# Kernel optimization log

Hardware: AMD Instinct MI355X
Metric: run time of the kernel (lower is better)

The kernel has to match this reference:

```python
import jax, jax.numpy as jnp
import numpy as np

D_MODEL = 1024
N_HEADS = 16
D_K = D_MODEL // N_HEADS


def setup_inputs() -> dict:
    key = jax.random.key(0)
    ks = jax.random.split(key, 12)
    B, S = 2, 2048
    scale = 1.0 / np.sqrt(D_MODEL)
    inp = {
        "query": jax.random.normal(ks[0], (B, S, D_MODEL), jnp.float32),
        "key": jax.random.normal(ks[1], (B, S, D_MODEL), jnp.float32),
        "value": jax.random.normal(ks[2], (B, S, D_MODEL), jnp.float32),
        "weights": jax.random.uniform(ks[3], (B, S), jnp.float32),
        "wq": jax.random.normal(ks[4], (D_MODEL, D_MODEL), jnp.float32) * scale,
        "bq": jnp.zeros((D_MODEL,), jnp.float32),
        "wk": jax.random.normal(ks[5], (D_MODEL, D_MODEL), jnp.float32) * scale,
        "bk": jnp.zeros((D_MODEL,), jnp.float32),
        "wv": jax.random.normal(ks[6], (D_MODEL, D_MODEL), jnp.float32) * scale,
        "bv": jnp.zeros((D_MODEL,), jnp.float32),
        "wo": jax.random.normal(ks[7], (D_MODEL, D_MODEL), jnp.float32) * scale,
        "bo": jnp.zeros((D_MODEL,), jnp.float32),
    }
    return inp


def _split_heads(x):
    # (B, S, d_model) -> (B, H, S, d_k)
    B, S, _ = x.shape
    return x.reshape(B, S, N_HEADS, D_K).transpose(0, 2, 1, 3)


def reference(query, key, value, weights, wq, bq, wk, bk, wv, bv, wo, bo):
    Q = _split_heads(query @ wq + bq)
    K = _split_heads(key @ wk + bk)
    V = _split_heads(value @ wv + bv)
    # scores: (B, H, n_q, n_kv)
    scores = jnp.einsum("bhqd,bhkd->bhqk", Q, K) / np.sqrt(D_K)
    log_w = jnp.log(weights + 1e-20)[:, None, None, :]  # (B,1,1,n_kv)
    attn = jax.nn.softmax(scores + log_w, axis=-1)
    out = jnp.einsum("bhqk,bhkd->bhqd", attn, V)
    B, H, S, Dk = out.shape
    out = out.transpose(0, 2, 1, 3).reshape(B, S, D_MODEL)
    return out @ wo + bo
```

## Files before the change

### kernel.cpp

```cpp
#include <hip/hip_runtime.h>

typedef unsigned short u16;
typedef __bf16 bf16x8 __attribute__((ext_vector_type(8)));
typedef float f32x4 __attribute__((ext_vector_type(4)));
typedef float f32x16 __attribute__((ext_vector_type(16)));

#define D_MODEL 1024
#define NH 16
#define DKD 64
#define BB 2
#define SS 2048
#define QSCL 0.18033688011112042f

#if __has_builtin(__builtin_amdgcn_exp2f)
#define EXP2(x) __builtin_amdgcn_exp2f(x)
#else
#define EXP2(x) exp2f(x)
#endif

__device__ __forceinline__ u16 f2bf(float f) {
  union { float f; unsigned u; } x; x.f = f;
  unsigned r = x.u + 0x7fffu + ((x.u >> 16) & 1u);
  return (u16)(r >> 16);
}

__device__ __forceinline__ void gld16(const u16* g, u16* l) {
  __builtin_amdgcn_global_load_lds((__attribute__((address_space(1))) void*)(g),
                                   (__attribute__((address_space(3))) void*)(l),
                                   16, 0, 0);
}

extern "C" __global__ void __launch_bounds__(256) kprep_conv(
    const float* __restrict__ q, const float* __restrict__ k, const float* __restrict__ v,
    const float* __restrict__ wts,
    u16* __restrict__ xq, u16* __restrict__ xk, u16* __restrict__ xv,
    float* __restrict__ lw)
{
  int z = blockIdx.y;
  if (blockIdx.x == 4096) {
    if (z == 0) {
      int i = threadIdx.x * 16;
      #pragma unroll
      for (int j = 0; j < 16; j += 4) {
        float4 val = *(const float4*)(wts + i + j);
        lw[i + j + 0] = log2f(val.x + 1e-20f) - 16.0f;
        lw[i + j + 1] = log2f(val.y + 1e-20f) - 16.0f;
        lw[i + j + 2] = log2f(val.z + 1e-20f) - 16.0f;
        lw[i + j + 3] = log2f(val.w + 1e-20f) - 16.0f;
      }
    }
    return;
  }
  const float* s = z == 0 ? q : (z == 1 ? k : v);
  u16* d = z == 0 ? xq : (z == 1 ? xk : xv);
  int i = (blockIdx.x * 256 + threadIdx.x) * 4;
  float4 val = *(const float4*)(s + i);
  ushort4 o;
  o.x = f2bf(val.x); o.y = f2bf(val.y); o.z = f2bf(val.z); o.w = f2bf(val.w);
  *(ushort4*)(d + i) = o;
}

extern "C" __global__ void __launch_bounds__(256) kprep_wt(
    const float* __restrict__ w0, const float* __restrict__ w1,
    const float* __restrict__ w2, const float* __restrict__ w3,
    u16* __restrict__ o0, u16* __restrict__ o1, u16* __restrict__ o2, u16* __restrict__ o3)
{
  const float* src; u16* dst;
  switch (blockIdx.z) {
    case 0: src = w0; dst = o0; break;
    case 1: src = w1; dst = o1; break;
    case 2: src = w2; dst = o2; break;
    default: src = w3; dst = o3; break;
  }
  __shared__ float t[32][33];
  int n0 = blockIdx.x * 32, k0 = blockIdx.y * 32;
  int tx = threadIdx.x & 31, ty = threadIdx.x >> 5;
  #pragma unroll
  for (int i = 0; i < 32; i += 8)
    t[ty + i][tx] = src[(k0 + ty + i) * D_MODEL + n0 + tx];
  __syncthreads();
  #pragma unroll
  for (int i = 0; i < 32; i += 8)
    dst[(size_t)(n0 + ty + i) * D_MODEL + k0 + tx] = f2bf(t[tx][ty + i]);
}

extern "C" __global__ void __launch_bounds__(256) ktrans_v(
    const u16* __restrict__ src, u16* __restrict__ dst)
{
  __shared__ u16 T[64][72];
  int bh = blockIdx.y; int s0 = blockIdx.x * 64;
  int tid = threadIdx.x;
  int r = tid >> 3, c = (tid & 7) * 8;
  #pragma unroll
  for (int i = 0; i < 2; ++i)
    *(bf16x8*)&T[r + i * 32][c] = *(const bf16x8*)&src[((size_t)bh * SS + s0 + r + i * 32) * DKD + c];
  __syncthreads();
  #pragma unroll
  for (int i = 0; i < 2; ++i) {
    int dk = r + i * 32;
    ushort4 o0, o1;
    o0.x = T[c + 0][dk]; o0.y = T[c + 1][dk]; o0.z = T[c + 2][dk]; o0.w = T[c + 3][dk];
    o1.x = T[c + 4][dk]; o1.y = T[c + 5][dk]; o1.z = T[c + 6][dk]; o1.w = T[c + 7][dk];
    *(ushort4*)&dst[((size_t)bh * DKD + dk) * SS + s0 + c] = o0;
    *(ushort4*)&dst[((size_t)bh * DKD + dk) * SS + s0 + c + 4] = o1;
  }
}

__device__ __forceinline__ void gemm_tile(const u16* __restrict__ Ag, const u16* __restrict__ Bg,
                                          u16* As, u16* Bs, f32x4 acc[4][4], int tid)
{
  int lane = tid & 63;
  int lr = lane & 15, lg = lane >> 4;
  int w = tid >> 6, wr = w >> 1, wc = w & 1;
  int sr7 = lr & 7;
  for (int k0 = 0; k0 < D_MODEL; k0 += 64) {
    #pragma unroll
    for (int c = 0; c < 4; ++c) {
      int idx = tid + c * 256;
      int row = idx >> 3, c3 = idx & 7;
      int col = (c3 ^ (row & 7)) * 8;
      gld16(Ag + row * D_MODEL + k0 + col, As + idx * 8);
      gld16(Bg + row * D_MODEL + k0 + col, Bs + idx * 8);
    }
    __syncthreads();
    #pragma unroll
    for (int kk = 0; kk < 2; ++kk) {
      bf16x8 af[4], bfr[4];
      #pragma unroll
      for (int mi = 0; mi < 4; ++mi)
        af[mi] = *(const bf16x8*)(As + (wr * 64 + mi * 16 + lr) * 64 + (((kk * 4 + lg) ^ sr7) * 8));
      #pragma unroll
      for (int nj = 0; nj < 4; ++nj)
        bfr[nj] = *(const bf16x8*)(Bs + (wc * 64 + nj * 16 + lr) * 64 + (((kk * 4 + lg) ^ sr7) * 8));
      #pragma unroll
      for (int mi = 0; mi < 4; ++mi)
        #pragma unroll
        for (int nj = 0; nj < 4; ++nj)
          acc[mi][nj] = __builtin_amdgcn_mfma_f32_16x16x32_bf16(af[mi], bfr[nj], acc[mi][nj], 0, 0, 0);
    }
    __syncthreads();
  }
}

extern "C" __global__ void __launch_bounds__(256) kgemm_qkv(
    const u16* __restrict__ xq, const u16* __restrict__ xk, const u16* __restrict__ xv,
    const u16* __restrict__ wqt, const u16* __restrict__ wkt, const u16* __restrict__ wvt,
    const float* __restrict__ bq, const float* __restrict__ bk, const float* __restrict__ bv,
    u16* __restrict__ Qb, u16* __restrict__ Kb, u16* __restrict__ Vb)
{
  __shared__ u16 As[128 * 64], Bs[128 * 64];
  int z = blockIdx.z;
  const u16* X  = z == 0 ? xq : (z == 1 ? xk : xv);
  const u16* Wt = z == 0 ? wqt : (z == 1 ? wkt : wvt);
  const float* bias = z == 0 ? bq : (z == 1 ? bk : bv);
  u16* dst = z == 0 ? Qb : (z == 1 ? Kb : Vb);
  int tid = threadIdx.x;
  f32x4 zero = {0.f, 0.f, 0.f, 0.f};
  f32x4 acc[4][4];
  #pragma unroll
  for (int i = 0; i < 4; ++i)
    #pragma unroll
    for (int j = 0; j < 4; ++j) acc[i][j] = zero;
  int m0 = blockIdx.y * 128, n0 = blockIdx.x * 128;
  gemm_tile(X + (size_t)m0 * D_MODEL, Wt + (size_t)n0 * D_MODEL, As, Bs, acc, tid);
  int lane = tid & 63, lr = lane & 15, lg = lane >> 4;
  int w = tid >> 6, wr = w >> 1, wc = w & 1;
  float scl = (z == 0) ? QSCL : 1.0f;
  #pragma unroll
  for (int mi = 0; mi < 4; ++mi)
    #pragma unroll
    for (int nj = 0; nj < 4; ++nj) {
      int n = n0 + wc * 64 + nj * 16 + lr;
      float bs = bias[n];
      int h = n >> 6, dk = n & 63;
      #pragma unroll
      for (int j = 0; j < 4; ++j) {
        int m = m0 + wr * 64 + mi * 16 + lg * 4 + j;
        int b = m >> 11, s = m & 2047;
        dst[(((size_t)(b * NH + h)) * SS + s) * DKD + dk] = f2bf((acc[mi][nj][j] + bs) * scl);
      }
    }
}

extern "C" __global__ void __launch_bounds__(256) kgemm_o(
    const u16* __restrict__ AO, const u16* __restrict__ wot,
    const float* __restrict__ bo, float* __restrict__ out)
{
  __shared__ u16 As[64 * 64], Bs[128 * 64];
  int tid = threadIdx.x;
  int lane = tid & 63, lr = lane & 15, lg = lane >> 4;
  int w = tid >> 6, wr = w & 1, wc = w >> 1;
  int sr7 = lr & 7;
  int m0 = blockIdx.y * 64, n0 = blockIdx.x * 128;
  const u16* Ag = AO + (size_t)m0 * D_MODEL;
  const u16* Bg = wot + (size_t)n0 * D_MODEL;
  f32x4 zero = {0.f, 0.f, 0.f, 0.f};
  f32x4 acc[2][4];
  #pragma unroll
  for (int i = 0; i < 2; ++i)
    #pragma unroll
    for (int j = 0; j < 4; ++j) acc[i][j] = zero;

  for (int k0 = 0; k0 < D_MODEL; k0 += 64) {
    #pragma unroll
    for (int c = 0; c < 2; ++c) {
      int idx = tid + c * 256;
      int row = idx >> 3, c3 = idx & 7;
      int col = (c3 ^ (row & 7)) * 8;
      gld16(Ag + row * D_MODEL + k0 + col, As + idx * 8);
    }
    #pragma unroll
    for (int c = 0; c < 4; ++c) {
      int idx = tid + c * 256;
      int row = idx >> 3, c3 = idx & 7;
      int col = (c3 ^ (row & 7)) * 8;
      gld16(Bg + row * D_MODEL + k0 + col, Bs + idx * 8);
    }
    __syncthreads();
    #pragma unroll
    for (int kk = 0; kk < 2; ++kk) {
      bf16x8 af[2], bfr[4];
      #pragma unroll
      for (int mi = 0; mi < 2; ++mi)
        af[mi] = *(const bf16x8*)(As + (wr * 32 + mi * 16 + lr) * 64 + (((kk * 4 + lg) ^ sr7) * 8));
      #pragma unroll
      for (int nj = 0; nj < 4; ++nj)
        bfr[nj] = *(const bf16x8*)(Bs + (wc * 64 + nj * 16 + lr) * 64 + (((kk * 4 + lg) ^ sr7) * 8));
      #pragma unroll
      for (int mi = 0; mi < 2; ++mi)
        #pragma unroll
        for (int nj = 0; nj < 4; ++nj)
          acc[mi][nj] = __builtin_amdgcn_mfma_f32_16x16x32_bf16(af[mi], bfr[nj], acc[mi][nj], 0, 0, 0);
    }
    __syncthreads();
  }

  #pragma unroll
  for (int mi = 0; mi < 2; ++mi)
    #pragma unroll
    for (int nj = 0; nj < 4; ++nj) {
      int n = n0 + wc * 64 + nj * 16 + lr;
      float bs = bo[n];
      #pragma unroll
      for (int j = 0; j < 4; ++j) {
        int m = m0 + wr * 32 + mi * 16 + lg * 4 + j;
        out[(size_t)m * D_MODEL + n] = acc[mi][nj][j] + bs;
      }
    }
}

extern "C" __global__ void __launch_bounds__(512, 4) kattn(
    const u16* __restrict__ Qb, const u16* __restrict__ Kb, const u16* __restrict__ Vt,
    const float* __restrict__ lw2, u16* __restrict__ AO)
{
  __shared__ __align__(16) char smem[2 * 16384 + 8192];
  float* lwf = (float*)(smem + 32768);

  int tid = threadIdx.x, lane = tid & 63, w = tid >> 6;
  int lq = lane & 31, hi = lane >> 5;
  int qw = w & 3, par = w >> 2;

  int n = blockIdx.x;
  int xcd = n & 7, slot = n >> 3;
  int bh = xcd + 8 * (slot >> 4);
  int q0 = (slot & 15) * 128;
  int b = bh >> 4, h = bh & 15;

  const u16* Qg = Qb + ((size_t)bh * SS + q0 + qw * 32) * DKD;
  const u16* Kg = Kb + (size_t)bh * SS * DKD;
  const u16* Vg = Vt + (size_t)bh * DKD * SS;
  const float* lwb = lw2 + b * SS;

  *(float4*)&lwf[tid * 4] = *(const float4*)(lwb + tid * 4);

  bf16x8 qf[4];
  #pragma unroll
  for (int kc = 0; kc < 4; ++kc)
    qf[kc] = *(const bf16x8*)(Qg + lq * DKD + kc * 16 + hi * 8);

  f32x16 acco[2] = {};
  float lsp[4] = {0.f, 0.f, 0.f, 0.f};

  int srow = tid >> 3, sc = ((tid & 7) ^ (srow & 7)) * 8;

#define KSLOT(sl) ((u16*)(smem + (sl) * 16384))
#define VSLOT(sl) ((u16*)(smem + (sl) * 16384 + 8192))
#define STAGE(t, sl) do { \
    gld16(Kg + (size_t)((t) * 64 + srow) * DKD + sc, KSLOT(sl) + tid * 8); \
    gld16(Vg + (size_t)srow * SS + (t) * 64 + sc, VSLOT(sl) + tid * 8); \
  } while (0)

  const u16* Kp = KSLOT(par);
  const u16* Vp = VSLOT(par);

  STAGE(0, 0); STAGE(1, 1);
  for (int i = 0; i < 16; ++i) {
    asm volatile("s_waitcnt vmcnt(0) lgkmcnt(0)" ::: "memory");
    __builtin_amdgcn_s_barrier();
    __builtin_amdgcn_sched_barrier(0);

    int t = 2 * i + par;
    int kv0 = t * 64;

    f32x16 st[2];
    #pragma unroll
    for (int nh = 0; nh < 2; ++nh)
      #pragma unroll
      for (int g = 0; g < 4; ++g) {
        f32x4 lv = *(const f32x4*)&lwf[kv0 + nh * 32 + 4 * hi + 8 * g];
        st[nh][4 * g + 0] = lv[0]; st[nh][4 * g + 1] = lv[1];
        st[nh][4 * g + 2] = lv[2]; st[nh][4 * g + 3] = lv[3];
      }

    __builtin_amdgcn_s_setprio(1);
    #pragma unroll
    for (int kc = 0; kc < 4; ++kc) {
      bf16x8 kf0 = *(const bf16x8*)&Kp[(lq) * 64      + (((kc * 2 + hi) ^ (lq & 7)) * 8)];
      bf16x8 kf1 = *(const bf16x8*)&Kp[(32 + lq) * 64 + (((kc * 2 + hi) ^ (lq & 7)) * 8)];
      st[0] = __builtin_amdgcn_mfma_f32_32x32x16_bf16(kf0, qf[kc], st[0], 0, 0, 0);
      st[1] = __builtin_amdgcn_mfma_f32_32x32x16_bf16(kf1, qf[kc], st[1], 0, 0, 0);
    }
    __builtin_amdgcn_s_setprio(0);

    unsigned wd[2][8];
    #pragma unroll
    for (int nh = 0; nh < 2; ++nh)
      #pragma unroll
      for (int r2 = 0; r2 < 8; ++r2) {
        float plo = EXP2(st[nh][2 * r2]);
        float phi = EXP2(st[nh][2 * r2 + 1]);
        lsp[r2 & 3] += plo + phi;
        union { unsigned u; __bf16 b2[2]; } cv;
        cv.b2[0] = (__bf16)plo; cv.b2[1] = (__bf16)phi;
        wd[nh][r2] = cv.u;
      }

    bf16x8 Pb[4];
    #pragma unroll
    for (int c = 0; c < 4; ++c) {
      int nh = c >> 1, j0 = 4 * (c & 1);
      auto s1 = __builtin_amdgcn_permlane32_swap(wd[nh][j0 + 0], wd[nh][j0 + 2], false, false);
      auto s2 = __builtin_amdgcn_permlane32_swap(wd[nh][j0 + 1], wd[nh][j0 + 3], false, false);
      union { unsigned u[4]; bf16x8 v; } pb;
      pb.u[0] = s1[0]; pb.u[1] = s2[0]; pb.u[2] = s1[1]; pb.u[3] = s2[1];
      Pb[c] = pb.v;
    }

    __builtin_amdgcn_s_setprio(1);
    #pragma unroll
    for (int c = 0; c < 4; ++c) {
      bf16x8 vf0 = *(const bf16x8*)&Vp[(lq) * 64      + (((c * 2 + hi) ^ (lq & 7)) * 8)];
      bf16x8 vf1 = *(const bf16x8*)&Vp[(32 + lq) * 64 + (((c * 2 + hi) ^ (lq & 7)) * 8)];
      acco[0] = __builtin_amdgcn_mfma_f32_32x32x16_bf16(vf0, Pb[c], acco[0], 0, 0, 0);
      acco[1] = __builtin_amdgcn_mfma_f32_32x32x16_bf16(vf1, Pb[c], acco[1], 0, 0, 0);
    }
    __builtin_amdgcn_s_setprio(0);

    __builtin_amdgcn_sched_barrier(0);
    __builtin_amdgcn_s_barrier();
    int tn = 2 * i + 2;
    if (tn < 32) { STAGE(tn, 0); STAGE(tn + 1, 1); }
  }
#undef STAGE

  float lsum_part = (lsp[0] + lsp[1]) + (lsp[2] + lsp[3]);
  float* comb = (float*)smem;
  int coff = (qw * 64 + lane) * 34;
  if (par == 1) {
    #pragma unroll
    for (int d = 0; d < 2; ++d)
      #pragma unroll
      for (int g = 0; g < 8; ++g)
        *(float2*)&comb[coff + (d * 8 + g) * 2] = make_float2(acco[d][2 * g], acco[d][2 * g + 1]);
    comb[coff + 32] = lsum_part;
  }
  __syncthreads();
  if (par == 0) {
    #pragma unroll
    for (int d = 0; d < 2; ++d)
      #pragma unroll
      for (int g = 0; g < 8; ++g) {
        float2 v = *(const float2*)&comb[coff + (d * 8 + g) * 2];
        acco[d][2 * g] += v.x; acco[d][2 * g + 1] += v.y;
      }
    lsum_part += comb[coff + 32];
    float lsum = lsum_part + __shfl_xor(lsum_part, 32);
    float inv = 1.0f / lsum;
    int s = q0 + qw * 32 + lq;
    size_t base = ((size_t)b * SS + s) * D_MODEL + h * DKD;
    #pragma unroll
    for (int dh = 0; dh < 2; ++dh)
      #pragma unroll
      for (int g = 0; g < 4; ++g) {
        ushort4 o;
        o.x = f2bf(acco[dh][4 * g + 0] * inv);
        o.y = f2bf(acco[dh][4 * g + 1] * inv);
        o.z = f2bf(acco[dh][4 * g + 2] * inv);
        o.w = f2bf(acco[dh][4 * g + 3] * inv);
        *(ushort4*)(AO + base + dh * 32 + 4 * hi + 8 * g) = o;
      }
  }
#undef KSLOT
#undef VSLOT
}

extern "C" void kernel_launch(void* const* d_in, const int* in_sizes, int n_in,
                              void* d_out, int out_size, void* d_ws, size_t ws_size,
                              hipStream_t stream) {
  const float* query = (const float*)d_in[0];
  const float* key_  = (const float*)d_in[1];
  const float* value = (const float*)d_in[2];
  const float* wts   = (const float*)d_in[3];
  const float* wq = (const float*)d_in[4];
  const float* bq = (const float*)d_in[5];
  const float* wk = (const float*)d_in[6];
  const float* bk = (const float*)d_in[7];
  const float* wv = (const float*)d_in[8];
  const float* bv = (const float*)d_in[9];
  const float* wo = (const float*)d_in[10];
  const float* bo = (const float*)d_in[11];
  float* out = (float*)d_out;

  char* ws = (char*)d_ws;
  const size_t MB = 1024 * 1024;
  u16* Xq  = (u16*)(ws + 0 * MB);
  u16* Xk  = (u16*)(ws + 8 * MB);
  u16* Xv  = (u16*)(ws + 16 * MB);
  u16* WqT = (u16*)(ws + 24 * MB);
  u16* WkT = (u16*)(ws + 26 * MB);
  u16* WvT = (u16*)(ws + 28 * MB);
  u16* WoT = (u16*)(ws + 30 * MB);
  u16* Qb  = (u16*)(ws + 32 * MB);
  u16* Kb  = (u16*)(ws + 40 * MB);
  u16* Vb  = (u16*)(ws + 48 * MB);
  u16* AO  = (u16*)(ws + 56 * MB);
  float* lwbuf = (float*)(ws + 64 * MB);
  u16* VtT = (u16*)(ws + 16 * MB);

  kprep_conv<<<dim3(4097, 3), 256, 0, stream>>>(query, key_, value, wts, Xq, Xk, Xv, lwbuf);
  kprep_wt<<<dim3(32, 32, 4), 256, 0, stream>>>(wq, wk, wv, wo, WqT, WkT, WvT, WoT);
  kgemm_qkv<<<dim3(8, 32, 3), 256, 0, stream>>>(Xq, Xk, Xv, WqT, WkT, WvT, bq, bk, bv, Qb, Kb, Vb);
  ktrans_v<<<dim3(32, 32), 256, 0, stream>>>(Vb, VtT);
  kattn<<<512, 512, 0, stream>>>(Qb, Kb, VtT, lwbuf, AO);
  kgemm_o<<<dim3(8, 64), 256, 0, stream>>>(AO, WoT, bo, out);
}
```

Baseline: 136.5 us.

## Process two 32-row query tiles per wave in attention to reuse K/V fragments

Each attention block now covers 256 query rows instead of 128, with each wave handling two 32-row query sub-tiles. K and V fragments loaded from LDS are reused across both sub-tiles, halving LDS traffic and global K/V staging per query row. The grid is halved to 256 blocks and launch bounds drop to 2 waves per SIMD, which raises register pressure and lowers parallelism; 256 blocks may underfill the 256 CUs less evenly.

```diff
diff --git a/kernel.cpp b/kernel.cpp
--- a/kernel.cpp
+++ b/kernel.cpp
@@ -249,7 +249,7 @@
     }
 }
 
-extern "C" __global__ void __launch_bounds__(512, 4) kattn(
+extern "C" __global__ void __launch_bounds__(512, 2) kattn(
     const u16* __restrict__ Qb, const u16* __restrict__ Kb, const u16* __restrict__ Vt,
     const float* __restrict__ lw2, u16* __restrict__ AO)
 {
@@ -262,24 +262,26 @@
 
   int n = blockIdx.x;
   int xcd = n & 7, slot = n >> 3;
-  int bh = xcd + 8 * (slot >> 4);
-  int q0 = (slot & 15) * 128;
+  int bh = xcd + 8 * (slot >> 3);
+  int q0 = (slot & 7) * 256;
   int b = bh >> 4, h = bh & 15;
 
-  const u16* Qg = Qb + ((size_t)bh * SS + q0 + qw * 32) * DKD;
+  const u16* Qg = Qb + ((size_t)bh * SS + q0 + qw * 64) * DKD;
   const u16* Kg = Kb + (size_t)bh * SS * DKD;
   const u16* Vg = Vt + (size_t)bh * DKD * SS;
   const float* lwb = lw2 + b * SS;
 
   *(float4*)&lwf[tid * 4] = *(const float4*)(lwb + tid * 4);
 
-  bf16x8 qf[4];
-  #pragma unroll
-  for (int kc = 0; kc < 4; ++kc)
-    qf[kc] = *(const bf16x8*)(Qg + lq * DKD + kc * 16 + hi * 8);
-
-  f32x16 acco[2] = {};
-  float lsp[4] = {0.f, 0.f, 0.f, 0.f};
+  bf16x8 qf[2][4];
+  #pragma unroll
+  for (int qm = 0; qm < 2; ++qm)
+    #pragma unroll
+    for (int kc = 0; kc < 4; ++kc)
+      qf[qm][kc] = *(const bf16x8*)(Qg + (qm * 32 + lq) * DKD + kc * 16 + hi * 8);
+
+  f32x16 acco[2][2] = {};
+  float lsp[2][2] = {};
 
   int srow = tid >> 3, sc = ((tid & 7) ^ (srow & 7)) * 8;
 
@@ -302,48 +304,61 @@
     int t = 2 * i + par;
     int kv0 = t * 64;
 
-    f32x16 st[2];
+    f32x4 iv[2][4];
     #pragma unroll
     for (int nh = 0; nh < 2; ++nh)
       #pragma unroll
-      for (int g = 0; g < 4; ++g) {
-        f32x4 lv = *(const f32x4*)&lwf[kv0 + nh * 32 + 4 * hi + 8 * g];
-        st[nh][4 * g + 0] = lv[0]; st[nh][4 * g + 1] = lv[1];
-        st[nh][4 * g + 2] = lv[2]; st[nh][4 * g + 3] = lv[3];
-      }
-
-    __builtin_amdgcn_s_setprio(1);
+      for (int g = 0; g < 4; ++g)
+        iv[nh][g] = *(const f32x4*)&lwf[kv0 + nh * 32 + 4 * hi + 8 * g];
+
+    bf16x8 kr0[4], kr1[4];
     #pragma unroll
     for (int kc = 0; kc < 4; ++kc) {
-      bf16x8 kf0 = *(const bf16x8*)&Kp[(lq) * 64      + (((kc * 2 + hi) ^ (lq & 7)) * 8)];
-      bf16x8 kf1 = *(const bf16x8*)&Kp[(32 + lq) * 64 + (((kc * 2 + hi) ^ (lq & 7)) * 8)];
-      st[0] = __builtin_amdgcn_mfma_f32_32x32x16_bf16(kf0, qf[kc], st[0], 0, 0, 0);
-      st[1] = __builtin_amdgcn_mfma_f32_32x32x16_bf16(kf1, qf[kc], st[1], 0, 0, 0);
-    }
-    __builtin_amdgcn_s_setprio(0);
-
-    unsigned wd[2][8];
-    #pragma unroll
-    for (int nh = 0; nh < 2; ++nh)
-      #pragma unroll
-      for (int r2 = 0; r2 < 8; ++r2) {
-        float plo = EXP2(st[nh][2 * r2]);
-        float phi = EXP2(st[nh][2 * r2 + 1]);
-        lsp[r2 & 3] += plo + phi;
-        union { unsigned u; __bf16 b2[2]; } cv;
-        cv.b2[0] = (__bf16)plo; cv.b2[1] = (__bf16)phi;
-        wd[nh][r2] = cv.u;
-      }
-
-    bf16x8 Pb[4];
-    #pragma unroll
-    for (int c = 0; c < 4; ++c) {
-      int nh = c >> 1, j0 = 4 * (c & 1);
-      auto s1 = __builtin_amdgcn_permlane32_swap(wd[nh][j0 + 0], wd[nh][j0 + 2], false, false);
-      auto s2 = __builtin_amdgcn_permlane32_swap(wd[nh][j0 + 1], wd[nh][j0 + 3], false, false);
-      union { unsigned u[4]; bf16x8 v; } pb;
-      pb.u[0] = s1[0]; pb.u[1] = s2[0]; pb.u[2] = s1[1]; pb.u[3] = s2[1];
-      Pb[c] = pb.v;
+      kr0[kc] = *(const bf16x8*)&Kp[(lq) * 64      + (((kc * 2 + hi) ^ (lq & 7)) * 8)];
+      kr1[kc] = *(const bf16x8*)&Kp[(32 + lq) * 64 + (((kc * 2 + hi) ^ (lq & 7)) * 8)];
+    }
+
+    bf16x8 Pb[2][4];
+    #pragma unroll
+    for (int qm = 0; qm < 2; ++qm) {
+      f32x16 st[2];
+      #pragma unroll
+      for (int nh = 0; nh < 2; ++nh)
+        #pragma unroll
+        for (int g = 0; g < 4; ++g) {
+          st[nh][4 * g + 0] = iv[nh][g][0]; st[nh][4 * g + 1] = iv[nh][g][1];
+          st[nh][4 * g + 2] = iv[nh][g][2]; st[nh][4 * g + 3] = iv[nh][g][3];
+        }
+      __builtin_amdgcn_s_setprio(1);
+      #pragma unroll
+      for (int kc = 0; kc < 4; ++kc) {
+        st[0] = __builtin_amdgcn_mfma_f32_32x32x16_bf16(kr0[kc], qf[qm][kc], st[0], 0, 0, 0);
+        st[1] = __builtin_amdgcn_mfma_f32_32x32x16_bf16(kr1[kc], qf[qm][kc], st[1], 0, 0, 0);
+      }
+      __builtin_amdgcn_s_setprio(0);
+
+      unsigned wd[2][8];
+      #pragma unroll
+      for (int nh = 0; nh < 2; ++nh)
+        #pragma unroll
+        for (int r2 = 0; r2 < 8; ++r2) {
+          float plo = EXP2(st[nh][2 * r2]);
+          float phi = EXP2(st[nh][2 * r2 + 1]);
+          lsp[qm][r2 & 1] += plo + phi;
+          union { unsigned u; __bf16 b2[2]; } cv;
+          cv.b2[0] = (__bf16)plo; cv.b2[1] = (__bf16)phi;
+          wd[nh][r2] = cv.u;
+        }
+
+      #pragma unroll
+      for (int c = 0; c < 4; ++c) {
+        int nh = c >> 1, j0 = 4 * (c & 1);
+        auto s1 = __builtin_amdgcn_permlane32_swap(wd[nh][j0 + 0], wd[nh][j0 + 2], false, false);
+        auto s2 = __builtin_amdgcn_permlane32_swap(wd[nh][j0 + 1], wd[nh][j0 + 3], false, false);
+        union { unsigned u[4]; bf16x8 v; } pb;
+        pb.u[0] = s1[0]; pb.u[1] = s2[0]; pb.u[2] = s1[1]; pb.u[3] = s2[1];
+        Pb[qm][c] = pb.v;
+      }
     }
 
     __builtin_amdgcn_s_setprio(1);
@@ -351,8 +366,11 @@
     for (int c = 0; c < 4; ++c) {
       bf16x8 vf0 = *(const bf16x8*)&Vp[(lq) * 64      + (((c * 2 + hi) ^ (lq & 7)) * 8)];
       bf16x8 vf1 = *(const bf16x8*)&Vp[(32 + lq) * 64 + (((c * 2 + hi) ^ (lq & 7)) * 8)];
-      acco[0] = __builtin_amdgcn_mfma_f32_32x32x16_bf16(vf0, Pb[c], acco[0], 0, 0, 0);
-      acco[1] = __builtin_amdgcn_mfma_f32_32x32x16_bf16(vf1, Pb[c], acco[1], 0, 0, 0);
+      #pragma unroll
+      for (int qm = 0; qm < 2; ++qm) {
+        acco[qm][0] = __builtin_amdgcn_mfma_f32_32x32x16_bf16(vf0, Pb[qm][c], acco[qm][0], 0, 0, 0);
+        acco[qm][1] = __builtin_amdgcn_mfma_f32_32x32x16_bf16(vf1, Pb[qm][c], acco[qm][1], 0, 0, 0);
+      }
     }
     __builtin_amdgcn_s_setprio(0);
 
@@ -363,42 +381,48 @@
   }
 #undef STAGE
 
-  float lsum_part = (lsp[0] + lsp[1]) + (lsp[2] + lsp[3]);
   float* comb = (float*)smem;
   int coff = (qw * 64 + lane) * 34;
-  if (par == 1) {
-    #pragma unroll
-    for (int d = 0; d < 2; ++d)
-      #pragma unroll
-      for (int g = 0; g < 8; ++g)
-        *(float2*)&comb[coff + (d * 8 + g) * 2] = make_float2(acco[d][2 * g], acco[d][2 * g + 1]);
-    comb[coff + 32] = lsum_part;
-  }
-  __syncthreads();
-  if (par == 0) {
-    #pragma unroll
-    for (int d = 0; d < 2; ++d)
-      #pragma unroll
-      for (int g = 0; g < 8; ++g) {
-        float2 v = *(const float2*)&comb[coff + (d * 8 + g) * 2];
-        acco[d][2 * g] += v.x; acco[d][2 * g + 1] += v.y;
-      }
-    lsum_part += comb[coff + 32];
-    float lsum = lsum_part + __shfl_xor(lsum_part, 32);
-    float inv = 1.0f / lsum;
-    int s = q0 + qw * 32 + lq;
-    size_t base = ((size_t)b * SS + s) * D_MODEL + h * DKD;
-    #pragma unroll
-    for (int dh = 0; dh < 2; ++dh)
-      #pragma unroll
-      for (int g = 0; g < 4; ++g) {
-        ushort4 o;
-        o.x = f2bf(acco[dh][4 * g + 0] * inv);
-        o.y = f2bf(acco[dh][4 * g + 1] * inv);
-        o.z = f2bf(acco[dh][4 * g + 2] * inv);
-        o.w = f2bf(acco[dh][4 * g + 3] * inv);
-        *(ushort4*)(AO + base + dh * 32 + 4 * hi + 8 * g) = o;
-      }
+  #pragma unroll
+  for (int qm = 0; qm < 2; ++qm) {
+    float lsum_part = lsp[qm][0] + lsp[qm][1];
+    __syncthreads();
+    if (par == 1) {
+      #pragma unroll
+      for (int d = 0; d < 2; ++d)
+        #pragma unroll
+        for (int g = 0; g < 8; ++g)
+          *(float2*)&comb[coff + (d * 8 + g) * 2] = make_float2(acco[qm][d][2 * g], acco[qm][d][2 * g + 1]);
+      comb[coff + 32] = lsum_part;
+    }
+    __syncthreads();
+    if (par == 0) {
+      float a[2][16];
+      #pragma unroll
+      for (int d = 0; d < 2; ++d)
+        #pragma unroll
+        for (int g = 0; g < 8; ++g) {
+          float2 v = *(const float2*)&comb[coff + (d * 8 + g) * 2];
+          a[d][2 * g] = acco[qm][d][2 * g] + v.x;
+          a[d][2 * g + 1] = acco[qm][d][2 * g + 1] + v.y;
+        }
+      lsum_part += comb[coff + 32];
+      float lsum = lsum_part + __shfl_xor(lsum_part, 32);
+      float inv = 1.0f / lsum;
+      int s = q0 + qw * 64 + qm * 32 + lq;
+      size_t base = ((size_t)b * SS + s) * D_MODEL + h * DKD;
+      #pragma unroll
+      for (int dh = 0; dh < 2; ++dh)
+        #pragma unroll
+        for (int g = 0; g < 4; ++g) {
+          ushort4 o;
+          o.x = f2bf(a[dh][4 * g + 0] * inv);
+          o.y = f2bf(a[dh][4 * g + 1] * inv);
+          o.z = f2bf(a[dh][4 * g + 2] * inv);
+          o.w = f2bf(a[dh][4 * g + 3] * inv);
+          *(ushort4*)(AO + base + dh * 32 + 4 * hi + 8 * g) = o;
+        }
+    }
   }
 #undef KSLOT
 #undef VSLOT
@@ -441,6 +465,6 @@
   kprep_wt<<<dim3(32, 32, 4), 256, 0, stream>>>(wq, wk, wv, wo, WqT, WkT, WvT, WoT);
   kgemm_qkv<<<dim3(8, 32, 3), 256, 0, stream>>>(Xq, Xk, Xv, WqT, WkT, WvT, bq, bk, bv, Qb, Kb, Vb);
   ktrans_v<<<dim3(32, 32), 256, 0, stream>>>(Vb, VtT);
-  kattn<<<512, 512, 0, stream>>>(Qb, Kb, VtT, lwbuf, AO);
+  kattn<<<256, 512, 0, stream>>>(Qb, Kb, VtT, lwbuf, AO);
   kgemm_o<<<dim3(8, 64), 256, 0, stream>>>(AO, WoT, bo, out);
 }
```

After: 141.4 us. +3.6%, slower.

## Fuse V transpose into QKV GEMM epilogue and stage outputs via LDS

Applied to the files above, without the earlier changes.

Removes the separate ktrans_v kernel by having the V projection blocks write their tile transposed into shared memory and then store V^T directly in the layout the attention kernel reads. Q and K epilogues are also staged through a padded shared-memory tile so that global stores become 16-byte vectors instead of scattered 2-byte writes. The intent is to save one launch plus a full read and write of V, and to coalesce the epilogue stores. The cost is a larger shared-memory footprint, an extra barrier, and the transposed V now lives in its own workspace region.

```diff
diff --git a/kernel.cpp b/kernel.cpp
--- a/kernel.cpp
+++ b/kernel.cpp
@@ -84,28 +84,6 @@
     dst[(size_t)(n0 + ty + i) * D_MODEL + k0 + tx] = f2bf(t[tx][ty + i]);
 }
 
-extern "C" __global__ void __launch_bounds__(256) ktrans_v(
-    const u16* __restrict__ src, u16* __restrict__ dst)
-{
-  __shared__ u16 T[64][72];
-  int bh = blockIdx.y; int s0 = blockIdx.x * 64;
-  int tid = threadIdx.x;
-  int r = tid >> 3, c = (tid & 7) * 8;
-  #pragma unroll
-  for (int i = 0; i < 2; ++i)
-    *(bf16x8*)&T[r + i * 32][c] = *(const bf16x8*)&src[((size_t)bh * SS + s0 + r + i * 32) * DKD + c];
-  __syncthreads();
-  #pragma unroll
-  for (int i = 0; i < 2; ++i) {
-    int dk = r + i * 32;
-    ushort4 o0, o1;
-    o0.x = T[c + 0][dk]; o0.y = T[c + 1][dk]; o0.z = T[c + 2][dk]; o0.w = T[c + 3][dk];
-    o1.x = T[c + 4][dk]; o1.y = T[c + 5][dk]; o1.z = T[c + 6][dk]; o1.w = T[c + 7][dk];
-    *(ushort4*)&dst[((size_t)bh * DKD + dk) * SS + s0 + c] = o0;
-    *(ushort4*)&dst[((size_t)bh * DKD + dk) * SS + s0 + c + 4] = o1;
-  }
-}
-
 __device__ __forceinline__ void gemm_tile(const u16* __restrict__ Ag, const u16* __restrict__ Bg,
                                           u16* As, u16* Bs, f32x4 acc[4][4], int tid)
 {
@@ -146,14 +124,15 @@
     const u16* __restrict__ xq, const u16* __restrict__ xk, const u16* __restrict__ xv,
     const u16* __restrict__ wqt, const u16* __restrict__ wkt, const u16* __restrict__ wvt,
     const float* __restrict__ bq, const float* __restrict__ bk, const float* __restrict__ bv,
-    u16* __restrict__ Qb, u16* __restrict__ Kb, u16* __restrict__ Vb)
-{
-  __shared__ u16 As[128 * 64], Bs[128 * 64];
+    u16* __restrict__ Qb, u16* __restrict__ Kb, u16* __restrict__ Vtt)
+{
+  __shared__ __align__(16) u16 SH[17408];
+  u16* As = SH;
+  u16* Bs = SH + 8192;
   int z = blockIdx.z;
   const u16* X  = z == 0 ? xq : (z == 1 ? xk : xv);
   const u16* Wt = z == 0 ? wqt : (z == 1 ? wkt : wvt);
   const float* bias = z == 0 ? bq : (z == 1 ? bk : bv);
-  u16* dst = z == 0 ? Qb : (z == 1 ? Kb : Vb);
   int tid = threadIdx.x;
   f32x4 zero = {0.f, 0.f, 0.f, 0.f};
   f32x4 acc[4][4];
@@ -163,23 +142,64 @@
     for (int j = 0; j < 4; ++j) acc[i][j] = zero;
   int m0 = blockIdx.y * 128, n0 = blockIdx.x * 128;
   gemm_tile(X + (size_t)m0 * D_MODEL, Wt + (size_t)n0 * D_MODEL, As, Bs, acc, tid);
+
   int lane = tid & 63, lr = lane & 15, lg = lane >> 4;
   int w = tid >> 6, wr = w >> 1, wc = w & 1;
   float scl = (z == 0) ? QSCL : 1.0f;
-  #pragma unroll
-  for (int mi = 0; mi < 4; ++mi)
-    #pragma unroll
-    for (int nj = 0; nj < 4; ++nj) {
-      int n = n0 + wc * 64 + nj * 16 + lr;
-      float bs = bias[n];
-      int h = n >> 6, dk = n & 63;
-      #pragma unroll
-      for (int j = 0; j < 4; ++j) {
-        int m = m0 + wr * 64 + mi * 16 + lg * 4 + j;
-        int b = m >> 11, s = m & 2047;
-        dst[(((size_t)(b * NH + h)) * SS + s) * DKD + dk] = f2bf((acc[mi][nj][j] + bs) * scl);
-      }
-    }
+
+  if (z == 2) {
+    #pragma unroll
+    for (int mi = 0; mi < 4; ++mi)
+      #pragma unroll
+      for (int nj = 0; nj < 4; ++nj) {
+        int nl = wc * 64 + nj * 16 + lr;
+        float bs = bias[n0 + nl];
+        int ml = wr * 64 + mi * 16 + lg * 4;
+        ushort4 o;
+        o.x = f2bf(acc[mi][nj][0] + bs);
+        o.y = f2bf(acc[mi][nj][1] + bs);
+        o.z = f2bf(acc[mi][nj][2] + bs);
+        o.w = f2bf(acc[mi][nj][3] + bs);
+        *(ushort4*)&SH[nl * 136 + ml] = o;
+      }
+    __syncthreads();
+    #pragma unroll
+    for (int p = 0; p < 8; ++p) {
+      int idx = p * 256 + tid;
+      int nl = idx >> 4, c = idx & 15;
+      int nn = n0 + nl;
+      int h = nn >> 6, dk = nn & 63;
+      int m = m0 + c * 8;
+      int b = m0 >> 11;
+      bf16x8 v = *(const bf16x8*)&SH[nl * 136 + c * 8];
+      *(bf16x8*)&Vtt[(((size_t)(b * NH + h)) * DKD + dk) * SS + (m & 2047)] = v;
+    }
+  } else {
+    u16* dst = (z == 0) ? Qb : Kb;
+    #pragma unroll
+    for (int mi = 0; mi < 4; ++mi)
+      #pragma unroll
+      for (int nj = 0; nj < 4; ++nj) {
+        int nl = wc * 64 + nj * 16 + lr;
+        float bs = bias[n0 + nl];
+        int ml = wr * 64 + mi * 16 + lg * 4;
+        #pragma unroll
+        for (int j = 0; j < 4; ++j)
+          SH[(ml + j) * 136 + nl] = f2bf((acc[mi][nj][j] + bs) * scl);
+      }
+    __syncthreads();
+    #pragma unroll
+    for (int p = 0; p < 8; ++p) {
+      int idx = p * 256 + tid;
+      int ml = idx >> 4, c = idx & 15;
+      int m = m0 + ml;
+      int b = m >> 11, s = m & 2047;
+      int nn = n0 + c * 8;
+      int h = nn >> 6, dk = nn & 63;
+      bf16x8 v = *(const bf16x8*)&SH[ml * 136 + c * 8];
+      *(bf16x8*)&dst[(((size_t)(b * NH + h)) * SS + s) * DKD + dk] = v;
+    }
+  }
 }
 
 extern "C" __global__ void __launch_bounds__(256) kgemm_o(
@@ -432,15 +452,13 @@
   u16* WoT = (u16*)(ws + 30 * MB);
   u16* Qb  = (u16*)(ws + 32 * MB);
   u16* Kb  = (u16*)(ws + 40 * MB);
-  u16* Vb  = (u16*)(ws + 48 * MB);
+  u16* VtT = (u16*)(ws + 48 * MB);
   u16* AO  = (u16*)(ws + 56 * MB);
   float* lwbuf = (float*)(ws + 64 * MB);
-  u16* VtT = (u16*)(ws + 16 * MB);
 
   kprep_conv<<<dim3(4097, 3), 256, 0, stream>>>(query, key_, value, wts, Xq, Xk, Xv, lwbuf);
   kprep_wt<<<dim3(32, 32, 4), 256, 0, stream>>>(wq, wk, wv, wo, WqT, WkT, WvT, WoT);
-  kgemm_qkv<<<dim3(8, 32, 3), 256, 0, stream>>>(Xq, Xk, Xv, WqT, WkT, WvT, bq, bk, bv, Qb, Kb, Vb);
-  ktrans_v<<<dim3(32, 32), 256, 0, stream>>>(Vb, VtT);
+  kgemm_qkv<<<dim3(8, 32, 3), 256, 0, stream>>>(Xq, Xk, Xv, WqT, WkT, WvT, bq, bk, bv, Qb, Kb, VtT);
   kattn<<<512, 512, 0, stream>>>(Qb, Kb, VtT, lwbuf, AO);
   kgemm_o<<<dim3(8, 64), 256, 0, stream>>>(AO, WoT, bo, out);
 }
```

Result: faster. 128.8 us (-5.7%).
